# Performance work log

Measured on AMD Instinct MI355X. Metric: run time of the kernel, lower is better.

The kernel has to match this reference:

```python
import jax, jax.numpy as jnp
import numpy as np

B, L, G, F = 64, 2048, 512, 3072
N = L + G + F            # nodes per graph
NT = B * N               # total flattened nodes
EG = 16384               # edges per graph (shared topology)
E = B * EG
H, D_IN, NUM_LAYERS = 64, 7, 4
EPS = 1e-5


def setup_inputs() -> dict:
    key = jax.random.key(0)
    ks = jax.random.split(key, 8)
    rng = np.random.default_rng(0)
    x = jax.random.normal(ks[0], (NT, D_IN), jnp.float32)
    # shared topology, replicated per graph with node offsets (PyG batched graph)
    eg = rng.integers(0, N, size=(2, EG))
    offs = (np.arange(B) * N)[None, :, None]
    edge_index = jnp.asarray((eg[:, None, :] + offs).reshape(2, E), dtype=jnp.int32)
    base = np.arange(B)[:, None] * N  # per-graph layout: [loc | gen | line]
    loc_idx = jnp.asarray((base + np.arange(0, L)[None, :]).reshape(-1), jnp.int32)
    prod_idx = jnp.asarray((base + np.arange(L, L + G)[None, :]).reshape(-1), jnp.int32)
    line_idx = jnp.asarray((base + np.arange(L + G, N)[None, :]).reshape(-1), jnp.int32)
    # gen->loc incidence [L, G]: each generator sits at one location
    gm = np.zeros((L, G), np.float32)
    gm[rng.integers(0, L, G), np.arange(G)] = 1.0
    # line->loc signed incidence [L, F]: +1 at from-bus, -1 at to-bus
    lm = np.zeros((L, F), np.float32)
    lm[rng.integers(0, L, F), np.arange(F)] += 1.0
    lm[rng.integers(0, L, F), np.arange(F)] -= 1.0
    s = 1.0 / np.sqrt(H)
    se = 1.0 / np.sqrt(D_IN)
    enc_w = jax.random.uniform(ks[1], (H, D_IN), jnp.float32, -se, se)
    enc_b = jnp.zeros((H,), jnp.float32)
    w_rel = jax.random.uniform(ks[2], (NUM_LAYERS, H, H), jnp.float32, -s, s)
    b_rel = jnp.zeros((NUM_LAYERS, H), jnp.float32)
    w_root = jax.random.uniform(ks[3], (NUM_LAYERS, H, H), jnp.float32, -s, s)
    ln_g = jnp.ones((H,), jnp.float32)
    ln_b = jnp.zeros((H,), jnp.float32)
    prod_w = jax.random.uniform(ks[4], (1, H), jnp.float32, -s, s)
    prod_b = jnp.zeros((1,), jnp.float32)
    flow_w = jax.random.uniform(ks[5], (1, H), jnp.float32, -s, s)
    flow_b = jnp.zeros((1,), jnp.float32)
    return {"x": x, "edge_index": edge_index, "prod_idx": prod_idx,
            "line_idx": line_idx, "loc_idx": loc_idx, "enc_w": enc_w, "enc_b": enc_b,
            "ln_g": ln_g, "ln_b": ln_b, "w_rel": w_rel, "b_rel": b_rel, "w_root": w_root,
            "prod_w": prod_w, "prod_b": prod_b, "flow_w": flow_w, "flow_b": flow_b,
            "gen_mask": jnp.asarray(gm), "line_mask": jnp.asarray(lm)}


def reference(x, edge_index, prod_idx, line_idx, loc_idx, enc_w, enc_b, ln_g, ln_b,
              w_rel, b_rel, w_root, prod_w, prod_b, flow_w, flow_b, gen_mask, line_mask):
    h = jax.nn.relu(x @ enc_w.T + enc_b)                       # [NT, H]
    src, dst = edge_index[0], edge_index[1]
    for i in range(NUM_LAYERS):
        # LayerNorm (shared across layers, as in the torch module)
        mu = jnp.mean(h, axis=-1, keepdims=True)
        var = jnp.mean((h - mu) ** 2, axis=-1, keepdims=True)
        hn = (h - mu) * jax.lax.rsqrt(var + EPS) * ln_g + ln_b
        # GraphConv: W_rel * sum_{j in N(i)} h_j + b_rel + W_root * h_i
        agg = jax.ops.segment_sum(hn[src], dst, num_segments=NT)  # gather + scatter-add
        h = jax.nn.relu(agg @ w_rel[i].T + b_rel[i] + hn @ w_root[i].T)
    p = (h[prod_idx] @ prod_w.T + prod_b).reshape(B, G)
    f = (h[line_idx] @ flow_w.T + flow_b).reshape(B, F)
    demand = x[loc_idx, 0].reshape(B, L)
    md = demand - (p @ gen_mask.T + f @ line_mask.T)           # unmet demand [B, L]
    return (p, f, md)
```

## Files before the change

kernel.cpp:

```cpp
#include <hip/hip_runtime.h>

#define B_ 64
#define L_ 2048
#define G_ 512
#define F_ 3072
#define N_ 5632
#define NT_ 360448
#define EG_ 16384
#define E_ 1048576
#define EPS_ 1e-5f
#define TCAP_ 384

typedef __attribute__((ext_vector_type(8))) short bf8v;
typedef __attribute__((ext_vector_type(4))) float f4v;

__device__ __forceinline__ unsigned short f2bf(float f){
  unsigned int u=__float_as_uint(f);
  unsigned int r=(u + 0x7fffu + ((u>>16)&1u))>>16;
  return (unsigned short)r;
}
__device__ __forceinline__ float bf2f(unsigned short h){
  return __uint_as_float(((unsigned int)h)<<16);
}

__global__ __launch_bounds__(256) void k_prep(const int* __restrict__ ei,
    unsigned short* __restrict__ wcat,
    const float* __restrict__ wrel, const float* __restrict__ wroot,
    int* __restrict__ offT, int* __restrict__ srcs2,
    const float* __restrict__ x, const int* __restrict__ loci, float* __restrict__ outmd,
    unsigned short* __restrict__ hn, const float* __restrict__ ew, const float* __restrict__ eb,
    const float* __restrict__ lng, const float* __restrict__ lnb,
    const float* __restrict__ gm, const float* __restrict__ lm,
    int* __restrict__ gloc, int* __restrict__ ffrom, int* __restrict__ fto){
  int bid=blockIdx.x, tid=threadIdx.x;
  if(bid>=6232){
    int gt=(bid-6232)*256+tid;
    {
      int base=gt*8;
      const float4* gp=(const float4*)(gm+base);
      float4 v0=gp[0], v1=gp[1];
      float vv[8]={v0.x,v0.y,v0.z,v0.w,v1.x,v1.y,v1.z,v1.w};
      #pragma unroll
      for(int j=0;j<8;j++) if(vv[j]!=0.f){
        int fi=base+j; int l=fi>>9; int g=fi&(G_-1);
        gloc[g]=l;
      }
      int base2=gt*48;
      const float4* lp=(const float4*)(lm+base2);
      #pragma unroll
      for(int q=0;q<12;q++){
        float4 v=lp[q];
        float uu[4]={v.x,v.y,v.z,v.w};
        #pragma unroll
        for(int j=0;j<4;j++) if(uu[j]!=0.f){
          int fi=base2+q*4+j; int l=fi/F_; int f=fi-l*F_;
          if(uu[j]>0.f) ffrom[f]=l; else fto[f]=l;
        }
      }
    }
    return;
  }
  if(bid>=600){
    int lane=tid&63, wid=tid>>6;
    int idx=bid-600;
    int gid=idx/88;
    int nb0=(idx%88)*64 + wid*16;
    int ng=lane>>4;
    int lig=lane&15;
    float w[4][7], bias[4], gam[4], bet[4];
    #pragma unroll
    for(int j=0;j<4;j++){
      int c=lig*4+j;
      #pragma unroll
      for(int k=0;k<7;k++) w[j][k]=ew[c*7+k];
      bias[j]=eb[c]; gam[j]=lng[c]; bet[j]=lnb[c];
    }
    #pragma unroll
    for(int t=0;t<4;t++){
      int n=nb0 + t*4 + ng;
      long xrow=((long)gid*N_+n)*7;
      float xv[7];
      #pragma unroll
      for(int k=0;k<7;k++) xv[k]=x[xrow+k];
      float h[4]; float s1=0.f, s2=0.f;
      #pragma unroll
      for(int j=0;j<4;j++){
        float a=bias[j];
        #pragma unroll
        for(int k=0;k<7;k++) a+=xv[k]*w[j][k];
        a=fmaxf(a,0.f);
        h[j]=a; s1+=a; s2+=a*a;
      }
      #pragma unroll
      for(int o=1;o<16;o<<=1){ s1+=__shfl_xor(s1,o,64); s2+=__shfl_xor(s2,o,64); }
      float mu=s1*(1.f/64.f);
      float var=s2*(1.f/64.f)-mu*mu;
      float inv=rsqrtf(var+EPS_);
      unsigned int p0=(unsigned int)f2bf((h[0]-mu)*inv*gam[0]+bet[0])
                    | ((unsigned int)f2bf((h[1]-mu)*inv*gam[1]+bet[1])<<16);
      unsigned int p1=(unsigned int)f2bf((h[2]-mu)*inv*gam[2]+bet[2])
                    | ((unsigned int)f2bf((h[3]-mu)*inv*gam[3]+bet[3])<<16);
      *(uint2*)(hn + (size_t)n*4096 + gid*64 + lig*4) = (uint2){p0,p1};
    }
    return;
  }
  if(bid>=88){
    int i=(bid-88)*256+tid;
    if(i<B_*L_) outmd[i]=x[(long)loci[i]*7];
    if(i<32768){
      int l=i>>13; int rest=i&8191; int n=rest>>7; int k=rest&127;
      float v=(k<64)? wrel[((long)l*64+n)*64+k] : wroot[((long)l*64+n)*64+(k-64)];
      wcat[i]=f2bf(v);
    }
    return;
  }
  __shared__ int cnt64[64], cur64[64];
  int nb=bid*64;
  if(tid<64) cnt64[tid]=0;
  __syncthreads();
  for(int e=tid;e<EG_;e+=1024){
    int d0=ei[E_+e], d1=ei[E_+e+256], d2=ei[E_+e+512], d3=ei[E_+e+768];
    unsigned t0=(unsigned)(d0-nb), t1=(unsigned)(d1-nb);
    unsigned t2=(unsigned)(d2-nb), t3=(unsigned)(d3-nb);
    if(t0<64u) atomicAdd(&cnt64[t0],1);
    if(t1<64u) atomicAdd(&cnt64[t1],1);
    if(t2<64u) atomicAdd(&cnt64[t2],1);
    if(t3<64u) atomicAdd(&cnt64[t3],1);
  }
  __syncthreads();
  if(tid<64){
    int v=cnt64[tid], s=v;
    #pragma unroll
    for(int o=1;o<64;o<<=1){ int u=__shfl_up(s,o,64); if(tid>=o) s+=u; }
    int ex=s-v;
    offT[bid*65+tid]=ex;
    cur64[tid]=ex;
    if(tid==63) offT[bid*65+64]=s;
  }
  __syncthreads();
  for(int e=tid;e<EG_;e+=1024){
    int s0=ei[e],    s1=ei[e+256],    s2=ei[e+512],    s3=ei[e+768];
    int d0=ei[E_+e], d1=ei[E_+e+256], d2=ei[E_+e+512], d3=ei[E_+e+768];
    unsigned t0=(unsigned)(d0-nb), t1=(unsigned)(d1-nb);
    unsigned t2=(unsigned)(d2-nb), t3=(unsigned)(d3-nb);
    if(t0<64u){ int p=atomicAdd(&cur64[t0],1); if(p<TCAP_) srcs2[bid*TCAP_+p]=s0|(d0<<16); }
    if(t1<64u){ int p=atomicAdd(&cur64[t1],1); if(p<TCAP_) srcs2[bid*TCAP_+p]=s1|(d1<<16); }
    if(t2<64u){ int p=atomicAdd(&cur64[t2],1); if(p<TCAP_) srcs2[bid*TCAP_+p]=s2|(d2<<16); }
    if(t3<64u){ int p=atomicAdd(&cur64[t3],1); if(p<TCAP_) srcs2[bid*TCAP_+p]=s3|(d3<<16); }
  }
}

__device__ __forceinline__ void upadd(float* a, uint4 qa, uint4 qb){
  unsigned int t[8]={qa.x,qa.y,qa.z,qa.w,qb.x,qb.y,qb.z,qb.w};
  #pragma unroll
  for(int j=0;j<8;j++){
    a[2*j]   += __uint_as_float(t[j]<<16);
    a[2*j+1] += __uint_as_float(t[j]&0xffff0000u);
  }
}

__device__ __forceinline__ void stw16(char* base, int r, int chunk, unsigned int p0,
                                      unsigned int p1, unsigned int p2, unsigned int p3){
  int byte = r*128 + chunk*16;
  byte ^= (r&7)<<4;
  *(uint4*)(base + byte) = (uint4){p0,p1,p2,p3};
}
__device__ __forceinline__ bf8v ld16(const char* base, int r, int chunk){
  int byte = r*128 + chunk*16;
  byte ^= (r&7)<<4;
  return *(const bf8v*)(base + byte);
}

__global__ __launch_bounds__(256,4) void k_layer(const unsigned short* __restrict__ hs,
    unsigned short* __restrict__ hd, const int* __restrict__ offT, const int* __restrict__ srcs2,
    const unsigned short* __restrict__ wcat, const float* __restrict__ brel,
    const float* __restrict__ lng, const float* __restrict__ lnb, int do_ln){
  __shared__ uint4 aggl4[512];
  char* agglc=(char*)aggl4;
  int tid=threadIdx.x;
  int w=tid>>6, lane=tid&63;
  int node=blockIdx.x;

  {
    int jj=node>>6, loc=node&63;
    int kb=offT[jj*65+loc];
    int ke=offT[jj*65+loc+1];
    const int* esp=srcs2 + jj*TCAP_;
    int co=tid*16;
    float aA[16];
    #pragma unroll
    for(int c=0;c<16;c++) aA[c]=0.f;
    int k=kb;
    for(; k+1<ke; k+=2){
      int u0=esp[k], u1=esp[k+1];
      const unsigned short* r0=hs+(size_t)(u0&0xffff)*4096+co;
      const unsigned short* r1=hs+(size_t)(u1&0xffff)*4096+co;
      uint4 qa0=*(const uint4*)r0, qb0=*(const uint4*)(r0+8);
      uint4 qa1=*(const uint4*)r1, qb1=*(const uint4*)(r1+8);
      upadd(aA,qa0,qb0);
      upadd(aA,qa1,qb1);
    }
    if(k<ke){
      int u0=esp[k];
      const unsigned short* r0=hs+(size_t)(u0&0xffff)*4096+co;
      uint4 qa0=*(const uint4*)r0, qb0=*(const uint4*)(r0+8);
      upadd(aA,qa0,qb0);
    }
    unsigned int pA[8];
    #pragma unroll
    for(int j=0;j<8;j++)
      pA[j]=(unsigned int)f2bf(aA[2*j]) | ((unsigned int)f2bf(aA[2*j+1])<<16);
    int rl=tid>>2, c2=(tid&3)*2;
    stw16(agglc, rl, c2,   pA[0],pA[1],pA[2],pA[3]);
    stw16(agglc, rl, c2+1, pA[4],pA[5],pA[6],pA[7]);
  }
  __syncthreads();

  int m=lane&15, quad=lane>>4;
  f4v acc[4];
  float bias_nt[4], g_nt[4], b_nt[4];
  #pragma unroll
  for(int nt=0;nt<4;nt++){
    int c=nt*16+m;
    bias_nt[nt]=brel[c];
    g_nt[nt]=lng[c]; b_nt[nt]=lnb[c];
    acc[nt]=(f4v){0.f,0.f,0.f,0.f};
  }
  {
    int R=w*16+m;
    bf8v af0=ld16(agglc,R,quad);
    bf8v af1=ld16(agglc,R,4+quad);
    const unsigned short* hrow=hs+(size_t)node*4096+R*64;
    bf8v af2=*(const bf8v*)(hrow+quad*8);
    bf8v af3=*(const bf8v*)(hrow+32+quad*8);
    #pragma unroll
    for(int nt=0;nt<4;nt++){
      const unsigned short* wrow=wcat + (long)(nt*16+m)*128 + quad*8;
      bf8v b0=*(const bf8v*)(wrow);
      bf8v b1=*(const bf8v*)(wrow+32);
      bf8v b2=*(const bf8v*)(wrow+64);
      bf8v b3=*(const bf8v*)(wrow+96);
      acc[nt]=__builtin_amdgcn_mfma_f32_16x16x32_bf16(af0,b0,acc[nt],0,0,0);
      acc[nt]=__builtin_amdgcn_mfma_f32_16x16x32_bf16(af1,b1,acc[nt],0,0,0);
      acc[nt]=__builtin_amdgcn_mfma_f32_16x16x32_bf16(af2,b2,acc[nt],0,0,0);
      acc[nt]=__builtin_amdgcn_mfma_f32_16x16x32_bf16(af3,b3,acc[nt],0,0,0);
    }
  }
  {
    float v[4][4];
    #pragma unroll
    for(int nt=0;nt<4;nt++)
      #pragma unroll
      for(int r=0;r<4;r++)
        v[nt][r]=fmaxf(acc[nt][r]+bias_nt[nt],0.f);
    if(do_ln){
      #pragma unroll
      for(int r=0;r<4;r++){
        float rs=v[0][r]+v[1][r]+v[2][r]+v[3][r];
        float rss=v[0][r]*v[0][r]+v[1][r]*v[1][r]+v[2][r]*v[2][r]+v[3][r]*v[3][r];
        #pragma unroll
        for(int o=1;o<16;o<<=1){ rs+=__shfl_xor(rs,o,64); rss+=__shfl_xor(rss,o,64); }
        float mu=rs*(1.f/64.f);
        float var=rss*(1.f/64.f)-mu*mu;
        float inv=rsqrtf(var+EPS_);
        #pragma unroll
        for(int nt=0;nt<4;nt++) v[nt][r]=(v[nt][r]-mu)*inv*g_nt[nt]+b_nt[nt];
      }
    }
    #pragma unroll
    for(int r=0;r<4;r++){
      int gg=w*16+quad*4+r;
      unsigned short* out=hd + (size_t)node*4096 + gg*64;
      #pragma unroll
      for(int nt=0;nt<4;nt++) out[nt*16+m]=f2bf(v[nt][r]);
    }
  }
}

__global__ __launch_bounds__(256) void k_readout2(const unsigned short* __restrict__ h,
    const int* __restrict__ prodi, const int* __restrict__ linei,
    const float* __restrict__ pw, const float* __restrict__ pb,
    const float* __restrict__ fw, const float* __restrict__ fb,
    float* __restrict__ outp, float* __restrict__ outf,
    const int* __restrict__ gloc, const int* __restrict__ ffrom, const int* __restrict__ fto,
    float* __restrict__ outmd){
  int i=blockIdx.x*256+threadIdx.x;
  const int MP=B_*G_;
  const int MT=MP+B_*F_;
  if(i>=MT) return;
  bool isp=i<MP;
  int j=isp? i : i-MP;
  unsigned nf=(unsigned)(isp? prodi[j] : linei[j]);
  unsigned gg=nf/(unsigned)N_;
  unsigned node=nf-gg*(unsigned)N_;
  const float* wv=isp? pw:fw;
  float acc=isp? pb[0]:fb[0];
  const uint4* hp=(const uint4*)(h + (size_t)node*4096 + gg*64);
  #pragma unroll
  for(int c=0;c<8;c++){
    uint4 u=hp[c];
    unsigned int uu[4]={u.x,u.y,u.z,u.w};
    #pragma unroll
    for(int q=0;q<4;q++){
      float lo=__uint_as_float(uu[q]<<16);
      float hi=__uint_as_float(uu[q]&0xffff0000u);
      acc += lo*wv[c*8+2*q] + hi*wv[c*8+2*q+1];
    }
  }
  if(isp){
    outp[j]=acc;
    int b=j/G_, g=j-(j/G_)*G_;
    int l=gloc[g];
    if(l>=0) atomicAdd(&outmd[(size_t)b*L_+l], -acc);
  }else{
    outf[j]=acc;
    int b=j/F_, f=j-(j/F_)*F_;
    int lf=ffrom[f], lt=fto[f];
    if(lf>=0) atomicAdd(&outmd[(size_t)b*L_+lf], -acc);
    if(lt>=0) atomicAdd(&outmd[(size_t)b*L_+lt],  acc);
  }
}

extern "C" void kernel_launch(void* const* d_in, const int* in_sizes, int n_in,
                              void* d_out, int out_size, void* d_ws, size_t ws_size,
                              hipStream_t stream){
  const float* x    =(const float*)d_in[0];
  const int*   ei   =(const int*)d_in[1];
  const int*   prodi=(const int*)d_in[2];
  const int*   linei=(const int*)d_in[3];
  const int*   loci =(const int*)d_in[4];
  const float* ew   =(const float*)d_in[5];
  const float* eb   =(const float*)d_in[6];
  const float* lng  =(const float*)d_in[7];
  const float* lnb  =(const float*)d_in[8];
  const float* wrel =(const float*)d_in[9];
  const float* brel =(const float*)d_in[10];
  const float* wroot=(const float*)d_in[11];
  const float* pw   =(const float*)d_in[12];
  const float* pb   =(const float*)d_in[13];
  const float* fw   =(const float*)d_in[14];
  const float* fb   =(const float*)d_in[15];
  const float* gm   =(const float*)d_in[16];
  const float* lm   =(const float*)d_in[17];

  char* ws=(char*)d_ws;
  unsigned short* hnA =(unsigned short*)ws;
  unsigned short* hnB =hnA + (size_t)NT_*64;
  unsigned short* wcat=hnB + (size_t)NT_*64;
  int* offT =(int*)(wcat + 32768);
  int* srcs2=offT + 88*65;
  int* gloc =srcs2 + 88*TCAP_;
  int* ffrom=gloc + G_;
  int* fto  =ffrom + F_;

  float* outp =(float*)d_out;
  float* outf =outp + (size_t)B_*G_;
  float* outmd=outf + (size_t)B_*F_;

  hipMemsetAsync(gloc, 0xFF, (G_+2*F_)*sizeof(int), stream);
  k_prep<<<600+NT_/64+512,256,0,stream>>>(ei,wcat,wrel,wroot,offT,srcs2,
                                      x,loci,outmd,hnA,ew,eb,lng,lnb,
                                      gm,lm,gloc,ffrom,fto);
  for(int i=0;i<4;i++){
    const unsigned short* hs=(i&1)?hnB:hnA;
    unsigned short* hd=(i&1)?hnA:hnB;
    k_layer<<<N_,256,0,stream>>>(hs,hd,offT,srcs2,wcat+(size_t)i*8192,
        brel+(size_t)i*64,lng,lnb,(i<3)?1:0);
  }
  {
    int MT=B_*(G_+F_);
    k_readout2<<<(MT+255)/256,256,0,stream>>>(hnA,prodi,linei,pw,pb,fw,fb,outp,outf,
                                              gloc,ffrom,fto,outmd);
  }
}
```

Baseline: 408.7 us.

## Process two destination nodes per layer block with padded edge lists

Each k_layer block now handles two adjacent destination nodes with 512 threads. Edge lists are padded per node pair to a multiple of four, using a zeroed dummy row at index N_, so the gather loop can be unrolled by four with no tail. Each thread gathers 8 features instead of 16 and routes each edge into one of two accumulators by destination. This adds more loads in flight and halves the block count. The costs are a per-edge branch, the extra padded dummy gathers, and an extra zero row in both h buffers.

After: 441.7 us. 1.08x slower.

```diff
diff --git a/kernel.cpp b/kernel.cpp
--- a/kernel.cpp
+++ b/kernel.cpp
@@ -10,6 +10,7 @@
 #define E_ 1048576
 #define EPS_ 1e-5f
 #define TCAP_ 384
+#define HROW_ 5633
 
 typedef __attribute__((ext_vector_type(8))) short bf8v;
 typedef __attribute__((ext_vector_type(4))) float f4v;
@@ -28,7 +29,8 @@
     const float* __restrict__ wrel, const float* __restrict__ wroot,
     int* __restrict__ offT, int* __restrict__ srcs2,
     const float* __restrict__ x, const int* __restrict__ loci, float* __restrict__ outmd,
-    unsigned short* __restrict__ hn, const float* __restrict__ ew, const float* __restrict__ eb,
+    unsigned short* __restrict__ hn, unsigned short* __restrict__ hnb,
+    const float* __restrict__ ew, const float* __restrict__ eb,
     const float* __restrict__ lng, const float* __restrict__ lnb,
     const float* __restrict__ gm, const float* __restrict__ lm,
     int* __restrict__ gloc, int* __restrict__ ffrom, int* __restrict__ fto){
@@ -111,6 +113,10 @@
       int l=i>>13; int rest=i&8191; int n=rest>>7; int k=rest&127;
       float v=(k<64)? wrel[((long)l*64+n)*64+k] : wroot[((long)l*64+n)*64+(k-64)];
       wcat[i]=f2bf(v);
+    }
+    if(i<4096){
+      hn [(size_t)N_*4096+i]=0;
+      hnb[(size_t)N_*4096+i]=0;
     }
     return;
   }
@@ -129,13 +135,27 @@
   }
   __syncthreads();
   if(tid<64){
-    int v=cnt64[tid], s=v;
+    int v=cnt64[tid];
+    int vo=__shfl_xor(v,1,64);
+    int c0=(tid&1)? vo : v;
+    int psum=v+vo;
+    int ppad=(psum+3)&~3;
+    int wv=(tid&1)? 0 : ppad;
+    int s=wv;
     #pragma unroll
     for(int o=1;o<64;o<<=1){ int u=__shfl_up(s,o,64); if(tid>=o) s+=u; }
-    int ex=s-v;
-    offT[bid*65+tid]=ex;
-    cur64[tid]=ex;
+    int pairstart=s-ppad;
+    int nst=pairstart + ((tid&1)? c0 : 0);
+    offT[bid*65+tid]=nst;
+    cur64[tid]=nst;
     if(tid==63) offT[bid*65+64]=s;
+    if(!(tid&1)){
+      int dw=N_ | ((nb+tid)<<16);
+      for(int q=psum;q<ppad;q++){
+        int p=pairstart+q;
+        if(p<TCAP_) srcs2[bid*TCAP_+p]=dw;
+      }
+    }
   }
   __syncthreads();
   for(int e=tid;e<EG_;e+=1024){
@@ -150,10 +170,10 @@
   }
 }
 
-__device__ __forceinline__ void upadd(float* a, uint4 qa, uint4 qb){
-  unsigned int t[8]={qa.x,qa.y,qa.z,qa.w,qb.x,qb.y,qb.z,qb.w};
+__device__ __forceinline__ void upadd8(float* a, uint4 q){
+  unsigned int t[4]={q.x,q.y,q.z,q.w};
   #pragma unroll
-  for(int j=0;j<8;j++){
+  for(int j=0;j<4;j++){
     a[2*j]   += __uint_as_float(t[j]<<16);
     a[2*j+1] += __uint_as_float(t[j]&0xffff0000u);
   }
@@ -171,48 +191,49 @@
   return *(const bf8v*)(base + byte);
 }
 
-__global__ __launch_bounds__(256,4) void k_layer(const unsigned short* __restrict__ hs,
+__global__ __launch_bounds__(512,4) void k_layer(const unsigned short* __restrict__ hs,
     unsigned short* __restrict__ hd, const int* __restrict__ offT, const int* __restrict__ srcs2,
     const unsigned short* __restrict__ wcat, const float* __restrict__ brel,
     const float* __restrict__ lng, const float* __restrict__ lnb, int do_ln){
-  __shared__ uint4 aggl4[512];
+  __shared__ uint4 aggl4[1024];
   char* agglc=(char*)aggl4;
   int tid=threadIdx.x;
   int w=tid>>6, lane=tid&63;
-  int node=blockIdx.x;
+  int dst0=blockIdx.x*2;
 
   {
-    int jj=node>>6, loc=node&63;
+    int jj=dst0>>6, loc=dst0&63;
     int kb=offT[jj*65+loc];
-    int ke=offT[jj*65+loc+1];
+    int ke=offT[jj*65+loc+2];
     const int* esp=srcs2 + jj*TCAP_;
-    int co=tid*16;
-    float aA[16];
-    #pragma unroll
-    for(int c=0;c<16;c++) aA[c]=0.f;
-    int k=kb;
-    for(; k+1<ke; k+=2){
-      int u0=esp[k], u1=esp[k+1];
+    int co=tid*8;
+    float aA[8], aB[8];
+    #pragma unroll
+    for(int c=0;c<8;c++){ aA[c]=0.f; aB[c]=0.f; }
+    for(int k=kb;k<ke;k+=4){
+      int u0=esp[k], u1=esp[k+1], u2=esp[k+2], u3=esp[k+3];
       const unsigned short* r0=hs+(size_t)(u0&0xffff)*4096+co;
       const unsigned short* r1=hs+(size_t)(u1&0xffff)*4096+co;
-      uint4 qa0=*(const uint4*)r0, qb0=*(const uint4*)(r0+8);
-      uint4 qa1=*(const uint4*)r1, qb1=*(const uint4*)(r1+8);
-      upadd(aA,qa0,qb0);
-      upadd(aA,qa1,qb1);
-    }
-    if(k<ke){
-      int u0=esp[k];
-      const unsigned short* r0=hs+(size_t)(u0&0xffff)*4096+co;
-      uint4 qa0=*(const uint4*)r0, qb0=*(const uint4*)(r0+8);
-      upadd(aA,qa0,qb0);
-    }
-    unsigned int pA[8];
-    #pragma unroll
-    for(int j=0;j<8;j++)
+      const unsigned short* r2=hs+(size_t)(u2&0xffff)*4096+co;
+      const unsigned short* r3=hs+(size_t)(u3&0xffff)*4096+co;
+      uint4 q0=*(const uint4*)r0;
+      uint4 q1=*(const uint4*)r1;
+      uint4 q2=*(const uint4*)r2;
+      uint4 q3=*(const uint4*)r3;
+      if((u0>>16)==dst0) upadd8(aA,q0); else upadd8(aB,q0);
+      if((u1>>16)==dst0) upadd8(aA,q1); else upadd8(aB,q1);
+      if((u2>>16)==dst0) upadd8(aA,q2); else upadd8(aB,q2);
+      if((u3>>16)==dst0) upadd8(aA,q3); else upadd8(aB,q3);
+    }
+    unsigned int pA[4], pB[4];
+    #pragma unroll
+    for(int j=0;j<4;j++){
       pA[j]=(unsigned int)f2bf(aA[2*j]) | ((unsigned int)f2bf(aA[2*j+1])<<16);
-    int rl=tid>>2, c2=(tid&3)*2;
-    stw16(agglc, rl, c2,   pA[0],pA[1],pA[2],pA[3]);
-    stw16(agglc, rl, c2+1, pA[4],pA[5],pA[6],pA[7]);
+      pB[j]=(unsigned int)f2bf(aB[2*j]) | ((unsigned int)f2bf(aB[2*j+1])<<16);
+    }
+    int rl=tid>>3, c=tid&7;
+    stw16(agglc, rl,    c, pA[0],pA[1],pA[2],pA[3]);
+    stw16(agglc, 64+rl, c, pB[0],pB[1],pB[2],pB[3]);
   }
   __syncthreads();
 
@@ -230,7 +251,8 @@
     int R=w*16+m;
     bf8v af0=ld16(agglc,R,quad);
     bf8v af1=ld16(agglc,R,4+quad);
-    const unsigned short* hrow=hs+(size_t)node*4096+R*64;
+    int dn=dst0+(R>>6), gg=R&63;
+    const unsigned short* hrow=hs+(size_t)dn*4096+gg*64;
     bf8v af2=*(const bf8v*)(hrow+quad*8);
     bf8v af3=*(const bf8v*)(hrow+32+quad*8);
     #pragma unroll
@@ -269,8 +291,9 @@
     }
     #pragma unroll
     for(int r=0;r<4;r++){
-      int gg=w*16+quad*4+r;
-      unsigned short* out=hd + (size_t)node*4096 + gg*64;
+      int R=w*16+quad*4+r;
+      int dn=dst0+(R>>6), gg=R&63;
+      unsigned short* out=hd + (size_t)dn*4096 + gg*64;
       #pragma unroll
       for(int nt=0;nt<4;nt++) out[nt*16+m]=f2bf(v[nt][r]);
     }
@@ -345,8 +368,8 @@
 
   char* ws=(char*)d_ws;
   unsigned short* hnA =(unsigned short*)ws;
-  unsigned short* hnB =hnA + (size_t)NT_*64;
-  unsigned short* wcat=hnB + (size_t)NT_*64;
+  unsigned short* hnB =hnA + (size_t)HROW_*4096;
+  unsigned short* wcat=hnB + (size_t)HROW_*4096;
   int* offT =(int*)(wcat + 32768);
   int* srcs2=offT + 88*65;
   int* gloc =srcs2 + 88*TCAP_;
@@ -359,12 +382,12 @@
 
   hipMemsetAsync(gloc, 0xFF, (G_+2*F_)*sizeof(int), stream);
   k_prep<<<600+NT_/64+512,256,0,stream>>>(ei,wcat,wrel,wroot,offT,srcs2,
-                                      x,loci,outmd,hnA,ew,eb,lng,lnb,
+                                      x,loci,outmd,hnA,hnB,ew,eb,lng,lnb,
                                       gm,lm,gloc,ffrom,fto);
   for(int i=0;i<4;i++){
     const unsigned short* hs=(i&1)?hnB:hnA;
     unsigned short* hd=(i&1)?hnA:hnB;
-    k_layer<<<N_,256,0,stream>>>(hs,hd,offT,srcs2,wcat+(size_t)i*8192,
+    k_layer<<<N_/2,512,0,stream>>>(hs,hd,offT,srcs2,wcat+(size_t)i*8192,
         brel+(size_t)i*64,lng,lnb,(i<3)?1:0);
   }
   {
```
